# Performance work log

Hardware: AMD Instinct MI355X
Metric: run time of the kernel (lower is better)

## Reference

```python
import jax, jax.numpy as jnp
import numpy as np
from jax import lax

B, S, D, H = 4, 1024, 1024, 16
DK = D // H


def setup_inputs() -> dict:
    key = jax.random.key(0)
    ks = jax.random.split(key, 8)
    s = 0.02
    return {
        "text_embeddings": jax.random.normal(ks[0], (B, S, D), jnp.float32),
        "text_mask": jnp.ones((B, S), jnp.int32),
        "W_G": jax.random.normal(ks[1], (D, D), jnp.float32) * s,
        "b_G": jnp.zeros((D,), jnp.float32),
        "Wq": jax.random.normal(ks[2], (D, D), jnp.float32) * s,
        "bq": jnp.zeros((D,), jnp.float32),
        "Wk": jax.random.normal(ks[3], (D, D), jnp.float32) * s,
        "bk": jnp.zeros((D,), jnp.float32),
        "conv_w": jax.random.normal(ks[4], (D, H, 3), jnp.float32) * s,
        "conv_b": jnp.zeros((D,), jnp.float32),
    }


def _rope_tables(seq_len, dk):
    # interleaved sinusoidal tables, each value repeated twice along feature dim
    pos = jnp.arange(seq_len, dtype=jnp.float32)[:, None]            # [S,1]
    inv = jnp.power(10000.0, -2.0 * jnp.arange(dk // 2, dtype=jnp.float32) / dk)
    ang = pos * inv                                                   # [S,DK/2]
    cos_pos = jnp.repeat(jnp.cos(ang), 2, axis=-1)[None, None]        # [1,1,S,DK]
    sin_pos = jnp.repeat(jnp.sin(ang), 2, axis=-1)[None, None]
    return cos_pos, sin_pos


def reference(text_embeddings, text_mask, W_G, b_G, Wq, bq, Wk, bk, conv_w, conv_b):
    b, s, d = text_embeddings.shape
    g = text_embeddings @ W_G + b_G                                   # [B,S,D]
    q = (g @ Wq + bq).reshape(b, s, H, DK).transpose(0, 2, 1, 3)      # [B,H,S,DK]
    k = (g @ Wk + bk).reshape(b, s, H, DK).transpose(0, 2, 1, 3)

    cos_pos, sin_pos = _rope_tables(s, DK)
    # NOTE: query rotation uses +q_odd (module does NOT negate for q), key uses -k_odd
    qw2 = jnp.stack([q[..., 1::2], q[..., ::2]], axis=-1).reshape(q.shape)
    qw = q * cos_pos + qw2 * sin_pos
    kw2 = jnp.stack([-k[..., 1::2], k[..., ::2]], axis=-1).reshape(k.shape)
    kw = k * cos_pos + kw2 * sin_pos

    scores = jnp.einsum("bhqd,bhkd->bhqk", qw, kw) / np.float32(np.sqrt(DK))
    mask = text_mask[:, None, None, :]                                # [B,1,1,S]
    scores = jnp.where(mask == 0, jnp.float32(-1e9), scores)
    p_attn = jax.nn.softmax(scores, axis=-1)                          # [B,H,S,S]

    row0 = p_attn[:, :, 0, :]                                         # [B,H,S]
    conv = lax.conv_general_dilated(
        row0, conv_w, window_strides=(1,), padding=[(1, 1)],
        dimension_numbers=("NCH", "OIH", "NCH"))                      # [B,D,S]
    return jax.nn.relu(conv + conv_b[None, :, None])
```

## Files before the change

kernel.cpp:

```cpp
#include <hip/hip_runtime.h>
#include <math.h>

#define B_  4
#define S_  1024
#define D_  1024
#define H_  16
#define DK_ 64
#define M_  (B_ * S_)

typedef __bf16 bf16x8 __attribute__((ext_vector_type(8)));
typedef float  f32x4  __attribute__((ext_vector_type(4)));

__device__ __forceinline__ unsigned short f2bf(float f) {
  unsigned u = __builtin_bit_cast(unsigned, f);
  u = (u + 0x7FFFu + ((u >> 16) & 1u)) >> 16;
  return (unsigned short)u;
}
__device__ __forceinline__ float bf2f(unsigned short h) {
  unsigned u = ((unsigned)h) << 16;
  return __builtin_bit_cast(float, u);
}

__device__ __forceinline__ void gl_lds16(const void* g, void* lds) {
  __builtin_amdgcn_global_load_lds(
      (const __attribute__((address_space(1))) unsigned int*)(unsigned long long)g,
      (__attribute__((address_space(3))) unsigned int*)(unsigned int)(unsigned long long)lds,
      16, 0, 0);
}

__global__ __launch_bounds__(256) void prep_kernel(
    const float* __restrict__ X, const float* __restrict__ W_G,
    const float* __restrict__ Wk, unsigned short* __restrict__ Xbf,
    unsigned short* __restrict__ WGT, unsigned short* __restrict__ WkT,
    float* __restrict__ tab) {
  __shared__ float tle[32][33];
  const int blk = blockIdx.x;
  const int tid = threadIdx.x;

  if (blk < 2048) {
    const int i = (blk * 256 + tid) * 2;
    const float4 v0 = ((const float4*)X)[i];
    const float4 v1 = ((const float4*)X)[i + 1];
    ushort4 h0, h1;
    h0.x = f2bf(v0.x); h0.y = f2bf(v0.y); h0.z = f2bf(v0.z); h0.w = f2bf(v0.w);
    h1.x = f2bf(v1.x); h1.y = f2bf(v1.y); h1.z = f2bf(v1.z); h1.w = f2bf(v1.w);
    ((ushort4*)Xbf)[i] = h0;
    ((ushort4*)Xbf)[i + 1] = h1;
  } else if (blk < 4096) {
    const bool isG = blk < 3072;
    const float* W = isG ? W_G : Wk;
    unsigned short* WT = isG ? WGT : WkT;
    const int t = isG ? blk - 2048 : blk - 3072;
    const int k0 = (t & 31) * 32;
    const int n0 = (t >> 5) * 32;
    const int tx = tid & 31;
    const int ty = tid >> 5;
#pragma unroll
    for (int r = 0; r < 32; r += 8)
      tle[ty + r][tx] = W[(size_t)(k0 + ty + r) * 1024 + n0 + tx];
    __syncthreads();
#pragma unroll
    for (int r = 0; r < 32; r += 8)
      WT[(size_t)(n0 + ty + r) * 1024 + k0 + tx] = f2bf(tle[tx][ty + r]);
  } else {
    const int idx = (blk - 4096) * 256 + tid;
    const int s = idx >> 5, j = idx & 31;
    const float inv = (float)exp(-(double)j * (9.210340371976182736 / 32.0));
    float sn, c;
    sincosf((float)s * inv, &sn, &c);
    tab[(size_t)s * 64 + 2 * j] = c;
    tab[(size_t)s * 64 + 2 * j + 1] = sn;
  }
}

#define GM 64
#define GN 128

__global__ __launch_bounds__(256) void gemm_bf16(
    const unsigned short* __restrict__ A, const unsigned short* __restrict__ BT,
    const float* __restrict__ bias, unsigned short* __restrict__ C,
    const float* __restrict__ Wq, float* __restrict__ part, int nGemmBlocks) {
  __shared__ __align__(16) unsigned short As[2][GM * 32];
  __shared__ __align__(16) unsigned short Bs[2][GN * 32];
  __shared__ float gs[4][32];

  const int flat = blockIdx.x;
  const int tid  = threadIdx.x;

  if (flat >= nGemmBlocks) {
    const int qb = flat - nGemmBlocks;
    const int slab = qb >> 2;
    const int n = (qb & 3) * 256 + tid;
    if (tid < 128) {
      const int b = tid >> 5, kk = tid & 31;
      gs[b][kk] = bf2f(A[(size_t)b * S_ * D_ + slab * 32 + kk]);
    }
    __syncthreads();
    float a0 = 0.f, a1 = 0.f, a2 = 0.f, a3 = 0.f;
#pragma unroll
    for (int kk = 0; kk < 32; ++kk) {
      const float w = Wq[(size_t)(slab * 32 + kk) * D_ + n];
      a0 = fmaf(gs[0][kk], w, a0);
      a1 = fmaf(gs[1][kk], w, a1);
      a2 = fmaf(gs[2][kk], w, a2);
      a3 = fmaf(gs[3][kk], w, a3);
    }
    part[(size_t)(slab * 4 + 0) * D_ + n] = a0;
    part[(size_t)(slab * 4 + 1) * D_ + n] = a1;
    part[(size_t)(slab * 4 + 2) * D_ + n] = a2;
    part[(size_t)(slab * 4 + 3) * D_ + n] = a3;
    return;
  }

  const int bx = flat >> 6;
  const int by = flat & 63;
  const int wv   = tid >> 6;
  const int lane = tid & 63;
  const int m0 = by * GM;
  const int n0 = bx * GN;

  const int colOff = (lane & 3) * 8;
  const size_t aOff  = (size_t)(m0 + 16 * wv + (lane >> 2)) * 1024 + colOff;
  const size_t bOff0 = (size_t)(n0 + 32 * wv + (lane >> 2)) * 1024 + colOff;
  const size_t bOff1 = bOff0 + (size_t)16 * 1024;

  const int l15  = lane & 15;
  const int quad = lane >> 4;

  f32x4 acc[4][2];
#pragma unroll
  for (int i = 0; i < 4; ++i)
#pragma unroll
    for (int j = 0; j < 2; ++j) acc[i][j] = (f32x4){0.f, 0.f, 0.f, 0.f};

#pragma unroll 1
  for (int k0 = 0; k0 < 1024; k0 += 64) {
    __syncthreads();
#pragma unroll
    for (int ks = 0; ks < 2; ++ks) {
      gl_lds16(A  + aOff  + k0 + ks * 32, &As[ks][wv * 512]);
      gl_lds16(BT + bOff0 + k0 + ks * 32, &Bs[ks][wv * 1024]);
      gl_lds16(BT + bOff1 + k0 + ks * 32, &Bs[ks][wv * 1024 + 512]);
    }
    __syncthreads();

#pragma unroll
    for (int ks = 0; ks < 2; ++ks) {
      bf16x8 af[4], bfr[2];
#pragma unroll
      for (int mi = 0; mi < 4; ++mi)
        af[mi] = *(const bf16x8*)(&As[ks][(mi * 16 + l15) * 32 + quad * 8]);
#pragma unroll
      for (int ni = 0; ni < 2; ++ni)
        bfr[ni] =
            *(const bf16x8*)(&Bs[ks][(wv * 32 + ni * 16 + l15) * 32 + quad * 8]);
#pragma unroll
      for (int mi = 0; mi < 4; ++mi)
#pragma unroll
        for (int ni = 0; ni < 2; ++ni)
          acc[mi][ni] = __builtin_amdgcn_mfma_f32_16x16x32_bf16(
              af[mi], bfr[ni], acc[mi][ni], 0, 0, 0);
    }
  }

#pragma unroll
  for (int ni = 0; ni < 2; ++ni) {
    const int n = n0 + wv * 32 + ni * 16 + l15;
    const float bv = bias[n];
#pragma unroll
    for (int mi = 0; mi < 4; ++mi) {
#pragma unroll
      for (int r = 0; r < 4; ++r) {
        const int m = m0 + mi * 16 + quad * 4 + r;
        C[(size_t)m * 1024 + n] = f2bf(acc[mi][ni][r] + bv);
      }
    }
  }
}

__global__ __launch_bounds__(256) void attn_scores_kernel(
    const unsigned short* __restrict__ Kbf, const float* __restrict__ part,
    const float* __restrict__ bq, const float* __restrict__ tab,
    const int* __restrict__ mask, float* __restrict__ scores,
    float* __restrict__ mS) {
  const int bi = blockIdx.x;
  const int b = bi >> 9;
  const int h = (bi >> 5) & 15;
  const int chunk = bi & 31;
  const int tid = threadIdx.x;
  const int bh = b * H_ + h;
  const int sl = tid >> 3;
  const int j  = tid & 7;
  const int s  = chunk * 32 + sl;

  __shared__ float q0s[DK_];
  __shared__ float wredm[4];
  __shared__ float wreds[4];

  if (tid < 64) {
    const int n = h * DK_ + tid;
    float v = bq[n];
#pragma unroll
    for (int sl2 = 0; sl2 < 32; ++sl2)
      v += part[(size_t)(sl2 * 4 + b) * D_ + n];
    q0s[tid] = v;
  }
  __syncthreads();

  const ushort4* kp =
      (const ushort4*)(Kbf + ((size_t)(b * S_ + s)) * D_ + h * DK_ + j * 8);
  const ushort4 k0 = kp[0], k1 = kp[1];
  const float4* tb = (const float4*)(tab + (size_t)s * 64 + j * 8);
  const float4 t0 = tb[0], t1 = tb[1];

  float dot = 0.f;
  {
    const float ka = bf2f(k0.x), kb = bf2f(k0.y);
    dot += q0s[j * 8 + 0] * (ka * t0.x - kb * t0.y) +
           q0s[j * 8 + 1] * (kb * t0.x + ka * t0.y);
  }
  {
    const float ka = bf2f(k0.z), kb = bf2f(k0.w);
    dot += q0s[j * 8 + 2] * (ka * t0.z - kb * t0.w) +
           q0s[j * 8 + 3] * (kb * t0.z + ka * t0.w);
  }
  {
    const float ka = bf2f(k1.x), kb = bf2f(k1.y);
    dot += q0s[j * 8 + 4] * (ka * t1.x - kb * t1.y) +
           q0s[j * 8 + 5] * (kb * t1.x + ka * t1.y);
  }
  {
    const float ka = bf2f(k1.z), kb = bf2f(k1.w);
    dot += q0s[j * 8 + 6] * (ka * t1.z - kb * t1.w) +
           q0s[j * 8 + 7] * (kb * t1.z + ka * t1.w);
  }
  dot += __shfl_xor(dot, 1);
  dot += __shfl_xor(dot, 2);
  dot += __shfl_xor(dot, 4);
  dot *= 0.125f;
  if (mask[b * S_ + s] == 0) dot = -1e9f;
  if (j == 0) scores[(size_t)bh * S_ + s] = dot;

  float mx = dot;
#pragma unroll
  for (int off = 8; off < 64; off <<= 1) mx = fmaxf(mx, __shfl_xor(mx, off));
  if ((tid & 63) == 0) wredm[tid >> 6] = mx;
  __syncthreads();
  mx = fmaxf(fmaxf(wredm[0], wredm[1]), fmaxf(wredm[2], wredm[3]));

  float e = (j == 0) ? expf(dot - mx) : 0.f;
#pragma unroll
  for (int off = 1; off < 64; off <<= 1) e += __shfl_xor(e, off);
  if ((tid & 63) == 0) wreds[tid >> 6] = e;
  __syncthreads();
  if (tid == 0) {
    mS[(size_t)(bh * 32 + chunk) * 2 + 0] = mx;
    mS[(size_t)(bh * 32 + chunk) * 2 + 1] =
        wreds[0] + wreds[1] + wreds[2] + wreds[3];
  }
}

__global__ __launch_bounds__(256) void conv_norm_relu_kernel(
    const float* __restrict__ scores, const float* __restrict__ mS,
    const float* __restrict__ cw, const float* __restrict__ cb,
    float* __restrict__ out) {
  const int b = blockIdx.y;
  const int s0 = blockIdx.x * 16;
  const int oz = blockIdx.z * 256;
  const int tid = threadIdx.x;

  __shared__ float msh[16], ish[16];
  __shared__ float sm[16][18];

  if (tid < 16) {
    const int bh = b * H_ + tid;
    float m = -3e38f;
#pragma unroll
    for (int c = 0; c < 32; ++c)
      m = fmaxf(m, mS[(size_t)(bh * 32 + c) * 2]);
    float S = 0.f;
#pragma unroll
    for (int c = 0; c < 32; ++c)
      S += mS[(size_t)(bh * 32 + c) * 2 + 1] *
           expf(mS[(size_t)(bh * 32 + c) * 2] - m);
    msh[tid] = m;
    ish[tid] = 1.f / S;
  }
  __syncthreads();

  for (int i = tid; i < 16 * 18; i += 256) {
    const int c = i / 18, ss = i % 18;
    const int gs = s0 - 1 + ss;
    float p = 0.f;
    if (gs >= 0 && gs < S_) {
      const int bh = b * H_ + c;
      p = expf(scores[(size_t)bh * S_ + gs] - msh[c]) * ish[c];
    }
    sm[c][ss] = p;
  }
  __syncthreads();

  const int og = tid >> 4;
  const int si = tid & 15;

  float r[16][3];
#pragma unroll
  for (int c = 0; c < 16; ++c) {
    r[c][0] = sm[c][si + 0];
    r[c][1] = sm[c][si + 1];
    r[c][2] = sm[c][si + 2];
  }

#pragma unroll 1
  for (int i = 0; i < 16; ++i) {
    const int o = oz + i * 16 + og;
    const float4* wo = (const float4*)(cw + (size_t)o * 48);
    float accv = cb[o];
#pragma unroll
    for (int q = 0; q < 12; ++q) {
      const float4 w4 = wo[q];
      const int f0 = q * 4;
      accv = fmaf(r[(f0 + 0) / 3][(f0 + 0) % 3], w4.x, accv);
      accv = fmaf(r[(f0 + 1) / 3][(f0 + 1) % 3], w4.y, accv);
      accv = fmaf(r[(f0 + 2) / 3][(f0 + 2) % 3], w4.z, accv);
      accv = fmaf(r[(f0 + 3) / 3][(f0 + 3) % 3], w4.w, accv);
    }
    out[((size_t)b * D_ + o) * S_ + s0 + si] = fmaxf(accv, 0.f);
  }
}

extern "C" void kernel_launch(void* const* d_in, const int* in_sizes, int n_in,
                              void* d_out, int out_size, void* d_ws,
                              size_t ws_size, hipStream_t stream) {
  const float* x    = (const float*)d_in[0];
  const int*   mask = (const int*)d_in[1];
  const float* W_G  = (const float*)d_in[2];
  const float* b_G  = (const float*)d_in[3];
  const float* Wq   = (const float*)d_in[4];
  const float* bq   = (const float*)d_in[5];
  const float* Wk   = (const float*)d_in[6];
  const float* bk   = (const float*)d_in[7];
  const float* cw   = (const float*)d_in[8];
  const float* cb   = (const float*)d_in[9];
  float* out = (float*)d_out;

  char* ws = (char*)d_ws;
  unsigned short* Xbf = (unsigned short*)(ws);
  unsigned short* G   = (unsigned short*)(ws + (8u << 20));
  unsigned short* Kbf = (unsigned short*)(ws + (16u << 20));
  unsigned short* WGT = (unsigned short*)(ws + (24u << 20));
  unsigned short* WkT = (unsigned short*)(ws + (26u << 20));
  float* part   = (float*)(ws + (28u << 20));
  float* ropeT  = (float*)(ws + (28u << 20) + (512u << 10));
  float* scores = (float*)(ws + (28u << 20) + (768u << 10));
  float* mS     = (float*)(ws + (28u << 20) + (1024u << 10));

  prep_kernel<<<4224, 256, 0, stream>>>(x, W_G, Wk, Xbf, WGT, WkT, ropeT);
  gemm_bf16<<<512, 256, 0, stream>>>(Xbf, WGT, b_G, G, nullptr, nullptr, 512);
  gemm_bf16<<<640, 256, 0, stream>>>(G, WkT, bk, Kbf, Wq, part, 512);
  attn_scores_kernel<<<2048, 256, 0, stream>>>(Kbf, part, bq, ropeT, mask,
                                               scores, mS);
  conv_norm_relu_kernel<<<dim3(S_ / 16, B_, 4), 256, 0, stream>>>(
      scores, mS, cw, cb, out);
}
```

Before: 160.4 us.

## Retile conv kernel to 64x64 output tiles with LDS-staged weights

Reworks the conv+softmax-normalize+relu kernel so each block covers 64 sequence positions by 64 output channels instead of 16 by 256. Conv weights and bias are staged once into LDS and read as wave-uniform broadcasts. Each wave now writes 64 contiguous floats per output row, where before it wrote scattered 16-float segments, which should coalesce the output stores. The trade-off is more LDS per block and a larger per-block prologue that loads the weights.

```diff
diff --git a/kernel.cpp b/kernel.cpp
--- a/kernel.cpp
+++ b/kernel.cpp
@@ -264,13 +264,15 @@
     const float* __restrict__ scores, const float* __restrict__ mS,
     const float* __restrict__ cw, const float* __restrict__ cb,
     float* __restrict__ out) {
-  const int b = blockIdx.y;
-  const int s0 = blockIdx.x * 16;
-  const int oz = blockIdx.z * 256;
+  const int b  = blockIdx.y;
+  const int s0 = blockIdx.x * 64;
+  const int o0 = blockIdx.z * 64;
   const int tid = threadIdx.x;
 
   __shared__ float msh[16], ish[16];
-  __shared__ float sm[16][18];
+  __shared__ __align__(16) float wsm[64 * 48];
+  __shared__ float cbs[64];
+  __shared__ float sm[16][66];
 
   if (tid < 16) {
     const int bh = b * H_ + tid;
@@ -286,46 +288,43 @@
     msh[tid] = m;
     ish[tid] = 1.f / S;
   }
-  __syncthreads();
-
-  for (int i = tid; i < 16 * 18; i += 256) {
-    const int c = i / 18, ss = i % 18;
+  for (int i = tid; i < 64 * 48; i += 256) wsm[i] = cw[(size_t)o0 * 48 + i];
+  if (tid < 64) cbs[tid] = cb[o0 + tid];
+  __syncthreads();
+
+  for (int i = tid; i < 16 * 66; i += 256) {
+    const int c = i / 66, ss = i % 66;
     const int gs = s0 - 1 + ss;
-    float p = 0.f;
-    if (gs >= 0 && gs < S_) {
-      const int bh = b * H_ + c;
-      p = expf(scores[(size_t)bh * S_ + gs] - msh[c]) * ish[c];
-    }
-    sm[c][ss] = p;
-  }
-  __syncthreads();
-
-  const int og = tid >> 4;
-  const int si = tid & 15;
-
+    sm[c][ss] = (gs >= 0 && gs < S_)
+                    ? expf(scores[(size_t)(b * H_ + c) * S_ + gs] - msh[c]) *
+                          ish[c]
+                    : 0.f;
+  }
+  __syncthreads();
+
+  const int w = tid >> 6;
+  const int l = tid & 63;
   float r[16][3];
 #pragma unroll
   for (int c = 0; c < 16; ++c) {
-    r[c][0] = sm[c][si + 0];
-    r[c][1] = sm[c][si + 1];
-    r[c][2] = sm[c][si + 2];
-  }
-
-#pragma unroll 1
+    r[c][0] = sm[c][l + 0];
+    r[c][1] = sm[c][l + 1];
+    r[c][2] = sm[c][l + 2];
+  }
+
+  float* outRow = out + ((size_t)b * D_ + o0) * S_ + s0 + l;
+#pragma unroll 2
   for (int i = 0; i < 16; ++i) {
-    const int o = oz + i * 16 + og;
-    const float4* wo = (const float4*)(cw + (size_t)o * 48);
-    float accv = cb[o];
-#pragma unroll
-    for (int q = 0; q < 12; ++q) {
-      const float4 w4 = wo[q];
-      const int f0 = q * 4;
-      accv = fmaf(r[(f0 + 0) / 3][(f0 + 0) % 3], w4.x, accv);
-      accv = fmaf(r[(f0 + 1) / 3][(f0 + 1) % 3], w4.y, accv);
-      accv = fmaf(r[(f0 + 2) / 3][(f0 + 2) % 3], w4.z, accv);
-      accv = fmaf(r[(f0 + 3) / 3][(f0 + 3) % 3], w4.w, accv);
-    }
-    out[((size_t)b * D_ + o) * S_ + s0 + si] = fmaxf(accv, 0.f);
+    const int ol = i * 4 + w;
+    const float* wr = &wsm[ol * 48];
+    float acc = cbs[ol];
+#pragma unroll
+    for (int c = 0; c < 16; ++c) {
+      acc = fmaf(r[c][0], wr[c * 3 + 0], acc);
+      acc = fmaf(r[c][1], wr[c * 3 + 1], acc);
+      acc = fmaf(r[c][2], wr[c * 3 + 2], acc);
+    }
+    outRow[(size_t)ol * S_] = fmaxf(acc, 0.f);
   }
 }
 
@@ -360,6 +359,6 @@
   gemm_bf16<<<640, 256, 0, stream>>>(G, WkT, bk, Kbf, Wq, part, 512);
   attn_scores_kernel<<<2048, 256, 0, stream>>>(Kbf, part, bq, ropeT, mask,
                                                scores, mS);
-  conv_norm_relu_kernel<<<dim3(S_ / 16, B_, 4), 256, 0, stream>>>(
+  conv_norm_relu_kernel<<<dim3(16, B_, 16), 256, 0, stream>>>(
       scores, mS, cw, cb, out);
 }
```

Result: faster. 157.1 us (-2.1%).
